# Performance work log

Hardware: AMD Instinct MI355X
Metric: run time of the kernel (lower is better)

The kernel has to match this reference:

```python
import math
import jax, jax.numpy as jnp
import numpy as np

B, L, S, H, E = 4, 2048, 2048, 8, 64

def setup_inputs() -> dict:
    key = jax.random.key(0)
    kq, kk, kv, km = jax.random.split(key, 4)
    queries = jax.random.normal(kq, (B, L, H, E), dtype=jnp.float32)
    keys = jax.random.normal(kk, (B, S, H, E), dtype=jnp.float32)
    values = jax.random.normal(kv, (B, S, H, E), dtype=jnp.float32)
    # bool mask [B, L, S]; True => masked out (filled with -10000)
    attn_mask = jax.random.randint(km, (B, L, S), 0, 2).astype(bool)
    return {"queries": queries, "keys": keys, "values": values, "attn_mask": attn_mask}

def reference(queries, keys, values, attn_mask):
    # queries: [B,L,H,E], keys/values: [B,S,H,E], attn_mask: [B,L,S] bool
    Edim = queries.shape[-1]
    scale = 1.0 / math.sqrt(Edim)  # self.scale is None -> 1/sqrt(E)
    scores = jnp.einsum('blhe,bshe->bhls', queries, keys) * scale  # [B,H,L,S]
    scores = jnp.where(attn_mask[:, None, :, :], jnp.float32(-10000.0), scores)
    A = jax.nn.softmax(scores, axis=-1)  # dropout is identity at eval time
    V = jnp.einsum('bhls,bshd->blhd', A, values)  # [B,L,H,E]
    return V, A
```

## Files before the change

kernel.cpp:

```cpp
#include <hip/hip_runtime.h>


typedef __attribute__((ext_vector_type(8))) short bf16x8;
typedef __attribute__((ext_vector_type(4))) short bf16x4;
typedef __attribute__((ext_vector_type(4))) float f32x4;

#define NB 4
#define NL 2048
#define NS 2048
#define NH 8
#define NE 64
#define SKC 64
#define SCALE 0.125f
#define MBIAS 4.0f

static __device__ __forceinline__ short f2bf(float x) {
  unsigned u = __builtin_bit_cast(unsigned, x);
  u += 0x7fffu + ((u >> 16) & 1u);
  return (short)(u >> 16);
}


__global__ __launch_bounds__(256) void cvt_headmajor(const float* __restrict__ in,
                                                     short* __restrict__ out) {
  long i4 = ((long)blockIdx.x * 256 + threadIdx.x) * 4;
  f32x4 v = *(const f32x4*)(in + i4);
  int e4 = (int)(i4 & 63);
  long r = i4 >> 6;
  int h = (int)(r & 7);
  long r2 = r >> 3;
  int t = (int)(r2 & 2047);
  int b = (int)(r2 >> 11);
  bf16x4 o;
  o[0] = f2bf(v[0]); o[1] = f2bf(v[1]); o[2] = f2bf(v[2]); o[3] = f2bf(v[3]);
  *(bf16x4*)(out + ((((long)b * NH + h) * NL + t) * NE + e4)) = o;
}

__global__ __launch_bounds__(256) void transpose_v(const float* __restrict__ V,
                                                   short* __restrict__ Vt) {
  __shared__ short t_lds[64 * 65];
  const int tid = threadIdx.x;
  const int b = blockIdx.x >> 8;
  const int h = (blockIdx.x >> 5) & 7;
  const int sb = (blockIdx.x & 31) * 64;
  {
    const int s = tid >> 2, e0 = (tid & 3) * 16;
    const float* vp = V + ((((long)b * NS + sb + s) * NH + h) * NE + e0);
    #pragma unroll
    for (int j = 0; j < 4; ++j) {
      f32x4 u = *(const f32x4*)(vp + j * 4);
      #pragma unroll
      for (int r = 0; r < 4; ++r) t_lds[(e0 + j * 4 + r) * 65 + s] = f2bf(u[r]);
    }
  }
  __syncthreads();
  {
    const int e = tid >> 2, s0 = (tid & 3) * 16;
    short* op = Vt + (((long)b * NH + h) * NE + e) * NS + sb + s0;
    short tmp[16];
    #pragma unroll
    for (int j = 0; j < 16; ++j) tmp[j] = t_lds[e * 65 + s0 + j];
    *(bf16x8*)(op)     = *(bf16x8*)(tmp);
    *(bf16x8*)(op + 8) = *(bf16x8*)(tmp + 8);
  }
}

__global__ __launch_bounds__(256) void pack_mask(const int* __restrict__ M,
                                                 unsigned long long* __restrict__ Mb) {
  const long total = (long)NB * NL * NS;
  long g = (long)blockIdx.x * 256 + threadIdx.x;
  const long stride = (long)gridDim.x * 256;
  for (; g < total; g += stride) {
    unsigned long long bal = __ballot(M[g] != 0);
    if ((threadIdx.x & 63) == 0) Mb[g >> 6] = bal;
  }
}


template<int RS>
static __device__ __forceinline__ void stage_tile(const short* __restrict__ base,
                                                  short* lds, int tid, int w) {
  #pragma unroll
  for (int c = 0; c < 2; ++c) {
    const int rr = (tid >> 3) + c * 32;
    const int gg = (tid & 7) ^ (rr & 7);
    const short* sp = base + (long)rr * RS + gg * 8;
    __builtin_amdgcn_global_load_lds(
        (const __attribute__((address_space(1))) void*)sp,
        (__attribute__((address_space(3))) void*)(void*)((char*)lds + c * 4096 + w * 1024),
        16, 0, 0);
  }
}

__global__ __launch_bounds__(256, 2)
void attn_main(const short* __restrict__ Qb, const short* __restrict__ Kb,
               const short* __restrict__ Vt, const unsigned long long* __restrict__ Mb,
               float* __restrict__ OutV, float* __restrict__ OutA)
{
  __shared__ short k_lds[2][SKC * 64];
  __shared__ short vt_lds[2][NE * 64];
  __shared__ short p_lds[4][16 * 64];

  const int bid = blockIdx.x;
  const int hh = bid & 7, qt = (bid >> 3) & 15, bb = bid >> 7;
  const int tid = threadIdx.x, w = tid >> 6, lane = tid & 63;
  const int lq = lane & 15, lg = lane >> 4;
  const int qwA = qt * 128 + w * 16, qrowA = qwA + lq;
  const int qwB = qwA + 64,          qrowB = qrowA + 64;

  const short* Kpan = Kb + (long)(bb * NH + hh) * NS * NE;
  const short* Vpan = Vt + (long)(bb * NH + hh) * NE * NS;

  bf16x8 qfA0, qfA1, qfB0, qfB1;
  {
    const short* qp = Qb + ((long)(bb * NH + hh) * NL + qrowA) * NE + 8 * lg;
    qfA0 = *(const bf16x8*)(qp);
    qfA1 = *(const bf16x8*)(qp + 32);
    qfB0 = *(const bf16x8*)(qp + 64 * NE);
    qfB1 = *(const bf16x8*)(qp + 64 * NE + 32);
  }

  const unsigned long long* mrowA = Mb + ((long)bb * NL + qrowA) * (NS / 64);
  const unsigned long long* mrowB = Mb + ((long)bb * NL + qrowB) * (NS / 64);

  float l0 = 0.f, l1 = 0.f, l2 = 0.f, l3 = 0.f;
  stage_tile<NE>(Kpan, &k_lds[0][0], tid, w);
  __syncthreads();
  unsigned long long mcA = mrowA[0];
  for (int sb = 0; sb < NS; sb += SKC) {
    const int cb = (sb >> 6) & 1;
    if (sb + SKC < NS)
      stage_tile<NE>(Kpan + (long)(sb + SKC) * NE, &k_lds[cb ^ 1][0], tid, w);
    const unsigned long long mnA = (sb + SKC < NS) ? mrowA[(sb >> 6) + 1] : 0ULL;
    #pragma unroll
    for (int st = 0; st < SKC; st += 16) {
      const int krow = st + lq, sw = (krow & 7) << 3;
      const bf16x8 kf0 = *(const bf16x8*)&k_lds[cb][(krow * 64 + 8 * lg) ^ sw];
      const bf16x8 kf1 = *(const bf16x8*)&k_lds[cb][(krow * 64 + 32 + 8 * lg) ^ sw];
      f32x4 c = {0.f, 0.f, 0.f, 0.f};
      c = __builtin_amdgcn_mfma_f32_16x16x32_bf16(kf0, qfA0, c, 0, 0, 0);
      c = __builtin_amdgcn_mfma_f32_16x16x32_bf16(kf1, qfA1, c, 0, 0, 0);
      const unsigned mb4 = (unsigned)(mcA >> (st + 4 * lg)) & 0xFu;
      l0 += (mb4 & 1u) ? 0.f : __expf(fmaf(c[0], SCALE, -MBIAS));
      l1 += (mb4 & 2u) ? 0.f : __expf(fmaf(c[1], SCALE, -MBIAS));
      l2 += (mb4 & 4u) ? 0.f : __expf(fmaf(c[2], SCALE, -MBIAS));
      l3 += (mb4 & 8u) ? 0.f : __expf(fmaf(c[3], SCALE, -MBIAS));
    }
    mcA = mnA;
    __syncthreads();
  }
  float lA = (l0 + l1) + (l2 + l3);
  lA += __shfl_xor(lA, 16, 64);
  lA += __shfl_xor(lA, 32, 64);
  const float rinvA = 1.0f / lA;

  f32x4 accvA[4];
  #pragma unroll
  for (int et = 0; et < 4; ++et) accvA[et] = (f32x4){0.f, 0.f, 0.f, 0.f};
  l0 = l1 = l2 = l3 = 0.f;

  float* arowA = OutA + (((long)(bb * NH + hh)) * NL + qrowA) * NS;

  stage_tile<NE>(Kpan, &k_lds[0][0], tid, w);
  stage_tile<NS>(Vpan, &vt_lds[0][0], tid, w);
  __syncthreads();
  mcA = mrowA[0];
  unsigned long long mcB = mrowB[0];
  for (int sb = 0; sb < NS; sb += SKC) {
    const int cb = (sb >> 6) & 1;
    if (sb + SKC < NS) {
      stage_tile<NE>(Kpan + (long)(sb + SKC) * NE, &k_lds[cb ^ 1][0], tid, w);
      stage_tile<NS>(Vpan + (sb + SKC), &vt_lds[cb ^ 1][0], tid, w);
    }
    const unsigned long long mnA = (sb + SKC < NS) ? mrowA[(sb >> 6) + 1] : 0ULL;
    const unsigned long long mnB = (sb + SKC < NS) ? mrowB[(sb >> 6) + 1] : 0ULL;
    #pragma unroll
    for (int st = 0; st < SKC; st += 16) {
      const int krow = st + lq, sw = (krow & 7) << 3;
      const bf16x8 kf0 = *(const bf16x8*)&k_lds[cb][(krow * 64 + 8 * lg) ^ sw];
      const bf16x8 kf1 = *(const bf16x8*)&k_lds[cb][(krow * 64 + 32 + 8 * lg) ^ sw];
      f32x4 cA = {0.f, 0.f, 0.f, 0.f};
      cA = __builtin_amdgcn_mfma_f32_16x16x32_bf16(kf0, qfA0, cA, 0, 0, 0);
      cA = __builtin_amdgcn_mfma_f32_16x16x32_bf16(kf1, qfA1, cA, 0, 0, 0);
      f32x4 cB = {0.f, 0.f, 0.f, 0.f};
      cB = __builtin_amdgcn_mfma_f32_16x16x32_bf16(kf0, qfB0, cB, 0, 0, 0);
      cB = __builtin_amdgcn_mfma_f32_16x16x32_bf16(kf1, qfB1, cB, 0, 0, 0);
      const unsigned mA4 = (unsigned)(mcA >> (st + 4 * lg)) & 0xFu;
      const float p0 = (mA4 & 1u) ? 0.f : __expf(fmaf(cA[0], SCALE, -MBIAS));
      const float p1 = (mA4 & 2u) ? 0.f : __expf(fmaf(cA[1], SCALE, -MBIAS));
      const float p2 = (mA4 & 4u) ? 0.f : __expf(fmaf(cA[2], SCALE, -MBIAS));
      const float p3 = (mA4 & 8u) ? 0.f : __expf(fmaf(cA[3], SCALE, -MBIAS));
      const float a0 = p0 * rinvA, a1 = p1 * rinvA, a2 = p2 * rinvA, a3 = p3 * rinvA;
      f32x4 av = {a0, a1, a2, a3};
      __builtin_nontemporal_store(av, (f32x4*)(arowA + sb + st + 4 * lg));
      bf16x4 pv;
      pv[0] = f2bf(a0); pv[1] = f2bf(a1); pv[2] = f2bf(a2); pv[3] = f2bf(a3);
      *(bf16x4*)&p_lds[w][(lq * 64 + st + 4 * lg) ^ ((lq & 7) << 3)] = pv;
      const unsigned mB4 = (unsigned)(mcB >> (st + 4 * lg)) & 0xFu;
      l0 += (mB4 & 1u) ? 0.f : __expf(fmaf(cB[0], SCALE, -MBIAS));
      l1 += (mB4 & 2u) ? 0.f : __expf(fmaf(cB[1], SCALE, -MBIAS));
      l2 += (mB4 & 4u) ? 0.f : __expf(fmaf(cB[2], SCALE, -MBIAS));
      l3 += (mB4 & 8u) ? 0.f : __expf(fmaf(cB[3], SCALE, -MBIAS));
    }
    #pragma unroll
    for (int kc2 = 0; kc2 < 2; ++kc2) {
      const bf16x8 pf = *(const bf16x8*)&p_lds[w][(lq * 64 + kc2 * 32 + 8 * lg) ^ ((lq & 7) << 3)];
      #pragma unroll
      for (int et = 0; et < 4; ++et) {
        const int er = et * 16 + lq;
        const bf16x8 vf = *(const bf16x8*)&vt_lds[cb][(er * 64 + kc2 * 32 + 8 * lg) ^ ((er & 7) << 3)];
        accvA[et] = __builtin_amdgcn_mfma_f32_16x16x32_bf16(pf, vf, accvA[et], 0, 0, 0);
      }
    }
    mcA = mnA; mcB = mnB;
    __syncthreads();
  }
  float lB = (l0 + l1) + (l2 + l3);
  lB += __shfl_xor(lB, 16, 64);
  lB += __shfl_xor(lB, 32, 64);
  const float rinvB = 1.0f / lB;

  {
    float* vout = OutV + (((long)bb * NL + qwA + 4 * lg) * NH + hh) * NE + lq;
    #pragma unroll
    for (int r = 0; r < 4; ++r)
      #pragma unroll
      for (int et = 0; et < 4; ++et)
        vout[(long)r * (NH * NE) + et * 16] = accvA[et][r];
  }

  f32x4 accvB[4];
  #pragma unroll
  for (int et = 0; et < 4; ++et) accvB[et] = (f32x4){0.f, 0.f, 0.f, 0.f};

  float* arowB = OutA + (((long)(bb * NH + hh)) * NL + qrowB) * NS;

  stage_tile<NE>(Kpan, &k_lds[0][0], tid, w);
  stage_tile<NS>(Vpan, &vt_lds[0][0], tid, w);
  __syncthreads();
  mcB = mrowB[0];
  for (int sb = 0; sb < NS; sb += SKC) {
    const int cb = (sb >> 6) & 1;
    if (sb + SKC < NS) {
      stage_tile<NE>(Kpan + (long)(sb + SKC) * NE, &k_lds[cb ^ 1][0], tid, w);
      stage_tile<NS>(Vpan + (sb + SKC), &vt_lds[cb ^ 1][0], tid, w);
    }
    const unsigned long long mnB = (sb + SKC < NS) ? mrowB[(sb >> 6) + 1] : 0ULL;
    #pragma unroll
    for (int st = 0; st < SKC; st += 16) {
      const int krow = st + lq, sw = (krow & 7) << 3;
      const bf16x8 kf0 = *(const bf16x8*)&k_lds[cb][(krow * 64 + 8 * lg) ^ sw];
      const bf16x8 kf1 = *(const bf16x8*)&k_lds[cb][(krow * 64 + 32 + 8 * lg) ^ sw];
      f32x4 c = {0.f, 0.f, 0.f, 0.f};
      c = __builtin_amdgcn_mfma_f32_16x16x32_bf16(kf0, qfB0, c, 0, 0, 0);
      c = __builtin_amdgcn_mfma_f32_16x16x32_bf16(kf1, qfB1, c, 0, 0, 0);
      const unsigned mb4 = (unsigned)(mcB >> (st + 4 * lg)) & 0xFu;
      const float p0 = (mb4 & 1u) ? 0.f : __expf(fmaf(c[0], SCALE, -MBIAS));
      const float p1 = (mb4 & 2u) ? 0.f : __expf(fmaf(c[1], SCALE, -MBIAS));
      const float p2 = (mb4 & 4u) ? 0.f : __expf(fmaf(c[2], SCALE, -MBIAS));
      const float p3 = (mb4 & 8u) ? 0.f : __expf(fmaf(c[3], SCALE, -MBIAS));
      const float a0 = p0 * rinvB, a1 = p1 * rinvB, a2 = p2 * rinvB, a3 = p3 * rinvB;
      f32x4 av = {a0, a1, a2, a3};
      __builtin_nontemporal_store(av, (f32x4*)(arowB + sb + st + 4 * lg));
      bf16x4 pv;
      pv[0] = f2bf(a0); pv[1] = f2bf(a1); pv[2] = f2bf(a2); pv[3] = f2bf(a3);
      *(bf16x4*)&p_lds[w][(lq * 64 + st + 4 * lg) ^ ((lq & 7) << 3)] = pv;
    }
    #pragma unroll
    for (int kc2 = 0; kc2 < 2; ++kc2) {
      const bf16x8 pf = *(const bf16x8*)&p_lds[w][(lq * 64 + kc2 * 32 + 8 * lg) ^ ((lq & 7) << 3)];
      #pragma unroll
      for (int et = 0; et < 4; ++et) {
        const int er = et * 16 + lq;
        const bf16x8 vf = *(const bf16x8*)&vt_lds[cb][(er * 64 + kc2 * 32 + 8 * lg) ^ ((er & 7) << 3)];
        accvB[et] = __builtin_amdgcn_mfma_f32_16x16x32_bf16(pf, vf, accvB[et], 0, 0, 0);
      }
    }
    mcB = mnB;
    __syncthreads();
  }

  {
    float* vout = OutV + (((long)bb * NL + qwB + 4 * lg) * NH + hh) * NE + lq;
    #pragma unroll
    for (int r = 0; r < 4; ++r)
      #pragma unroll
      for (int et = 0; et < 4; ++et)
        vout[(long)r * (NH * NE) + et * 16] = accvB[et][r];
  }
}

extern "C" void kernel_launch(void* const* d_in, const int* in_sizes, int n_in,
                              void* d_out, int out_size, void* d_ws, size_t ws_size,
                              hipStream_t stream) {
  const float* Q = (const float*)d_in[0];
  const float* K = (const float*)d_in[1];
  const float* V = (const float*)d_in[2];
  const int*   M = (const int*)d_in[3];
  float* outv = (float*)d_out;
  float* outa = outv + (size_t)NB * NL * NH * NE;

  const size_t NQK = (size_t)NB * NH * NL * NE;
  short* Qb  = (short*)d_ws;
  short* Kbw = Qb + NQK;
  short* Vtw = Kbw + NQK;
  unsigned long long* Mbp = (unsigned long long*)(Vtw + NQK);

  cvt_headmajor<<<dim3((unsigned)(NQK / 4 / 256)), 256, 0, stream>>>(Q, Qb);
  cvt_headmajor<<<dim3((unsigned)(NQK / 4 / 256)), 256, 0, stream>>>(K, Kbw);
  transpose_v<<<dim3(NB * NH * (NS / 64)), 256, 0, stream>>>(V, Vtw);
  pack_mask<<<dim3(2048), 256, 0, stream>>>(M, Mbp);

  attn_main<<<dim3(NB * (NL / 128) * NH), 256, 0, stream>>>(Qb, Kbw, Vtw, Mbp, outv, outa);
}
```

Measured before the change: 213.6 us.

## Fuse preprocessing into one kernel, load Q directly, use exp2

Merges the K conversion, V transpose and mask packing into a single launch partitioned by block index. It drops the separate Q conversion by having the main kernel read fp32 Q and pack it to bf16 in registers. It also replaces __expf with hardware exp2 using pre-scaled log2e constants. The aim is to cut launch overhead and one round trip through memory for Q, at the cost of slightly more register work at the start of the main kernel.

Result: faster. 203.1 us (-4.9%).

```diff
diff --git a/kernel.cpp b/kernel.cpp
--- a/kernel.cpp
+++ b/kernel.cpp
@@ -11,8 +11,9 @@
 #define NH 8
 #define NE 64
 #define SKC 64
-#define SCALE 0.125f
-#define MBIAS 4.0f
+#define SC2 0.18033688011112042f
+#define MB2 -5.770780163555854f
+#define EXP2(x) __builtin_amdgcn_exp2f(x)
 
 static __device__ __forceinline__ short f2bf(float x) {
   unsigned u = __builtin_bit_cast(unsigned, x);
@@ -20,59 +21,64 @@
   return (short)(u >> 16);
 }
 
-
-__global__ __launch_bounds__(256) void cvt_headmajor(const float* __restrict__ in,
-                                                     short* __restrict__ out) {
-  long i4 = ((long)blockIdx.x * 256 + threadIdx.x) * 4;
-  f32x4 v = *(const f32x4*)(in + i4);
-  int e4 = (int)(i4 & 63);
-  long r = i4 >> 6;
-  int h = (int)(r & 7);
-  long r2 = r >> 3;
-  int t = (int)(r2 & 2047);
-  int b = (int)(r2 >> 11);
-  bf16x4 o;
-  o[0] = f2bf(v[0]); o[1] = f2bf(v[1]); o[2] = f2bf(v[2]); o[3] = f2bf(v[3]);
-  *(bf16x4*)(out + ((((long)b * NH + h) * NL + t) * NE + e4)) = o;
-}
-
-__global__ __launch_bounds__(256) void transpose_v(const float* __restrict__ V,
-                                                   short* __restrict__ Vt) {
+static __device__ __forceinline__ bf16x8 pack8(f32x4 a, f32x4 b) {
+  bf16x8 t;
+  t[0] = f2bf(a[0]); t[1] = f2bf(a[1]); t[2] = f2bf(a[2]); t[3] = f2bf(a[3]);
+  t[4] = f2bf(b[0]); t[5] = f2bf(b[1]); t[6] = f2bf(b[2]); t[7] = f2bf(b[3]);
+  return t;
+}
+
+__global__ __launch_bounds__(256)
+void prep_all(const float* __restrict__ K, const float* __restrict__ V,
+              const int* __restrict__ M, short* __restrict__ Kb,
+              short* __restrict__ Vt, unsigned long long* __restrict__ Mb) {
   __shared__ short t_lds[64 * 65];
-  const int tid = threadIdx.x;
-  const int b = blockIdx.x >> 8;
-  const int h = (blockIdx.x >> 5) & 7;
-  const int sb = (blockIdx.x & 31) * 64;
-  {
-    const int s = tid >> 2, e0 = (tid & 3) * 16;
-    const float* vp = V + ((((long)b * NS + sb + s) * NH + h) * NE + e0);
-    #pragma unroll
-    for (int j = 0; j < 4; ++j) {
-      f32x4 u = *(const f32x4*)(vp + j * 4);
-      #pragma unroll
-      for (int r = 0; r < 4; ++r) t_lds[(e0 + j * 4 + r) * 65 + s] = f2bf(u[r]);
-    }
-  }
-  __syncthreads();
-  {
-    const int e = tid >> 2, s0 = (tid & 3) * 16;
-    short* op = Vt + (((long)b * NH + h) * NE + e) * NS + sb + s0;
-    short tmp[16];
-    #pragma unroll
-    for (int j = 0; j < 16; ++j) tmp[j] = t_lds[e * 65 + s0 + j];
-    *(bf16x8*)(op)     = *(bf16x8*)(tmp);
-    *(bf16x8*)(op + 8) = *(bf16x8*)(tmp + 8);
-  }
-}
-
-__global__ __launch_bounds__(256) void pack_mask(const int* __restrict__ M,
-                                                 unsigned long long* __restrict__ Mb) {
-  const long total = (long)NB * NL * NS;
-  long g = (long)blockIdx.x * 256 + threadIdx.x;
-  const long stride = (long)gridDim.x * 256;
-  for (; g < total; g += stride) {
-    unsigned long long bal = __ballot(M[g] != 0);
-    if ((threadIdx.x & 63) == 0) Mb[g >> 6] = bal;
+  const int bid = blockIdx.x, tid = threadIdx.x;
+  if (bid < 4096) {
+    long i4 = ((long)bid * 256 + tid) * 4;
+    f32x4 v = *(const f32x4*)(K + i4);
+    int e4 = (int)(i4 & 63);
+    long r = i4 >> 6;
+    int h = (int)(r & 7);
+    long r2 = r >> 3;
+    int t = (int)(r2 & 2047);
+    int b = (int)(r2 >> 11);
+    bf16x4 o;
+    o[0] = f2bf(v[0]); o[1] = f2bf(v[1]); o[2] = f2bf(v[2]); o[3] = f2bf(v[3]);
+    *(bf16x4*)(Kb + ((((long)b * NH + h) * NL + t) * NE + e4)) = o;
+  } else if (bid < 5120) {
+    const int vb = bid - 4096;
+    const int b = vb >> 8;
+    const int h = (vb >> 5) & 7;
+    const int sb = (vb & 31) * 64;
+    {
+      const int s = tid >> 2, e0 = (tid & 3) * 16;
+      const float* vp = V + ((((long)b * NS + sb + s) * NH + h) * NE + e0);
+      #pragma unroll
+      for (int j = 0; j < 4; ++j) {
+        f32x4 u = *(const f32x4*)(vp + j * 4);
+        #pragma unroll
+        for (int r = 0; r < 4; ++r) t_lds[(e0 + j * 4 + r) * 65 + s] = f2bf(u[r]);
+      }
+    }
+    __syncthreads();
+    {
+      const int e = tid >> 2, s0 = (tid & 3) * 16;
+      short* op = Vt + (((long)b * NH + h) * NE + e) * NS + sb + s0;
+      short tmp[16];
+      #pragma unroll
+      for (int j = 0; j < 16; ++j) tmp[j] = t_lds[e * 65 + s0 + j];
+      *(bf16x8*)(op)     = *(bf16x8*)(tmp);
+      *(bf16x8*)(op + 8) = *(bf16x8*)(tmp + 8);
+    }
+  } else {
+    const long total = (long)NB * NL * NS;
+    long g = (long)(bid - 5120) * 256 + tid;
+    const long stride = 2048L * 256;
+    for (; g < total; g += stride) {
+      unsigned long long bal = __ballot(M[g] != 0);
+      if ((tid & 63) == 0) Mb[g >> 6] = bal;
+    }
   }
 }
 
@@ -93,7 +99,7 @@
 }
 
 __global__ __launch_bounds__(256, 2)
-void attn_main(const short* __restrict__ Qb, const short* __restrict__ Kb,
+void attn_main(const float* __restrict__ Qg, const short* __restrict__ Kb,
                const short* __restrict__ Vt, const unsigned long long* __restrict__ Mb,
                float* __restrict__ OutV, float* __restrict__ OutA)
 {
@@ -113,11 +119,12 @@
 
   bf16x8 qfA0, qfA1, qfB0, qfB1;
   {
-    const short* qp = Qb + ((long)(bb * NH + hh) * NL + qrowA) * NE + 8 * lg;
-    qfA0 = *(const bf16x8*)(qp);
-    qfA1 = *(const bf16x8*)(qp + 32);
-    qfB0 = *(const bf16x8*)(qp + 64 * NE);
-    qfB1 = *(const bf16x8*)(qp + 64 * NE + 32);
+    const float* qp = Qg + (((long)bb * NL + qrowA) * NH + hh) * NE + 8 * lg;
+    qfA0 = pack8(*(const f32x4*)(qp),      *(const f32x4*)(qp + 4));
+    qfA1 = pack8(*(const f32x4*)(qp + 32), *(const f32x4*)(qp + 36));
+    const float* qpB = qp + (long)64 * NH * NE;
+    qfB0 = pack8(*(const f32x4*)(qpB),      *(const f32x4*)(qpB + 4));
+    qfB1 = pack8(*(const f32x4*)(qpB + 32), *(const f32x4*)(qpB + 36));
   }
 
   const unsigned long long* mrowA = Mb + ((long)bb * NL + qrowA) * (NS / 64);
@@ -141,10 +148,10 @@
       c = __builtin_amdgcn_mfma_f32_16x16x32_bf16(kf0, qfA0, c, 0, 0, 0);
       c = __builtin_amdgcn_mfma_f32_16x16x32_bf16(kf1, qfA1, c, 0, 0, 0);
       const unsigned mb4 = (unsigned)(mcA >> (st + 4 * lg)) & 0xFu;
-      l0 += (mb4 & 1u) ? 0.f : __expf(fmaf(c[0], SCALE, -MBIAS));
-      l1 += (mb4 & 2u) ? 0.f : __expf(fmaf(c[1], SCALE, -MBIAS));
-      l2 += (mb4 & 4u) ? 0.f : __expf(fmaf(c[2], SCALE, -MBIAS));
-      l3 += (mb4 & 8u) ? 0.f : __expf(fmaf(c[3], SCALE, -MBIAS));
+      l0 += (mb4 & 1u) ? 0.f : EXP2(fmaf(c[0], SC2, MB2));
+      l1 += (mb4 & 2u) ? 0.f : EXP2(fmaf(c[1], SC2, MB2));
+      l2 += (mb4 & 4u) ? 0.f : EXP2(fmaf(c[2], SC2, MB2));
+      l3 += (mb4 & 8u) ? 0.f : EXP2(fmaf(c[3], SC2, MB2));
     }
     mcA = mnA;
     __syncthreads();
@@ -186,10 +193,10 @@
       cB = __builtin_amdgcn_mfma_f32_16x16x32_bf16(kf0, qfB0, cB, 0, 0, 0);
       cB = __builtin_amdgcn_mfma_f32_16x16x32_bf16(kf1, qfB1, cB, 0, 0, 0);
       const unsigned mA4 = (unsigned)(mcA >> (st + 4 * lg)) & 0xFu;
-      const float p0 = (mA4 & 1u) ? 0.f : __expf(fmaf(cA[0], SCALE, -MBIAS));
-      const float p1 = (mA4 & 2u) ? 0.f : __expf(fmaf(cA[1], SCALE, -MBIAS));
-      const float p2 = (mA4 & 4u) ? 0.f : __expf(fmaf(cA[2], SCALE, -MBIAS));
-      const float p3 = (mA4 & 8u) ? 0.f : __expf(fmaf(cA[3], SCALE, -MBIAS));
+      const float p0 = (mA4 & 1u) ? 0.f : EXP2(fmaf(cA[0], SC2, MB2));
+      const float p1 = (mA4 & 2u) ? 0.f : EXP2(fmaf(cA[1], SC2, MB2));
+      const float p2 = (mA4 & 4u) ? 0.f : EXP2(fmaf(cA[2], SC2, MB2));
+      const float p3 = (mA4 & 8u) ? 0.f : EXP2(fmaf(cA[3], SC2, MB2));
       const float a0 = p0 * rinvA, a1 = p1 * rinvA, a2 = p2 * rinvA, a3 = p3 * rinvA;
       f32x4 av = {a0, a1, a2, a3};
       __builtin_nontemporal_store(av, (f32x4*)(arowA + sb + st + 4 * lg));
@@ -197,10 +204,10 @@
       pv[0] = f2bf(a0); pv[1] = f2bf(a1); pv[2] = f2bf(a2); pv[3] = f2bf(a3);
       *(bf16x4*)&p_lds[w][(lq * 64 + st + 4 * lg) ^ ((lq & 7) << 3)] = pv;
       const unsigned mB4 = (unsigned)(mcB >> (st + 4 * lg)) & 0xFu;
-      l0 += (mB4 & 1u) ? 0.f : __expf(fmaf(cB[0], SCALE, -MBIAS));
-      l1 += (mB4 & 2u) ? 0.f : __expf(fmaf(cB[1], SCALE, -MBIAS));
-      l2 += (mB4 & 4u) ? 0.f : __expf(fmaf(cB[2], SCALE, -MBIAS));
-      l3 += (mB4 & 8u) ? 0.f : __expf(fmaf(cB[3], SCALE, -MBIAS));
+      l0 += (mB4 & 1u) ? 0.f : EXP2(fmaf(cB[0], SC2, MB2));
+      l1 += (mB4 & 2u) ? 0.f : EXP2(fmaf(cB[1], SC2, MB2));
+      l2 += (mB4 & 4u) ? 0.f : EXP2(fmaf(cB[2], SC2, MB2));
+      l3 += (mB4 & 8u) ? 0.f : EXP2(fmaf(cB[3], SC2, MB2));
     }
     #pragma unroll
     for (int kc2 = 0; kc2 < 2; ++kc2) {
@@ -255,10 +262,10 @@
       c = __builtin_amdgcn_mfma_f32_16x16x32_bf16(kf0, qfB0, c, 0, 0, 0);
       c = __builtin_amdgcn_mfma_f32_16x16x32_bf16(kf1, qfB1, c, 0, 0, 0);
       const unsigned mb4 = (unsigned)(mcB >> (st + 4 * lg)) & 0xFu;
-      const float p0 = (mb4 & 1u) ? 0.f : __expf(fmaf(c[0], SCALE, -MBIAS));
-      const float p1 = (mb4 & 2u) ? 0.f : __expf(fmaf(c[1], SCALE, -MBIAS));
-      const float p2 = (mb4 & 4u) ? 0.f : __expf(fmaf(c[2], SCALE, -MBIAS));
-      const float p3 = (mb4 & 8u) ? 0.f : __expf(fmaf(c[3], SCALE, -MBIAS));
+      const float p0 = (mb4 & 1u) ? 0.f : EXP2(fmaf(c[0], SC2, MB2));
+      const float p1 = (mb4 & 2u) ? 0.f : EXP2(fmaf(c[1], SC2, MB2));
+      const float p2 = (mb4 & 4u) ? 0.f : EXP2(fmaf(c[2], SC2, MB2));
+      const float p3 = (mb4 & 8u) ? 0.f : EXP2(fmaf(c[3], SC2, MB2));
       const float a0 = p0 * rinvB, a1 = p1 * rinvB, a2 = p2 * rinvB, a3 = p3 * rinvB;
       f32x4 av = {a0, a1, a2, a3};
       __builtin_nontemporal_store(av, (f32x4*)(arowB + sb + st + 4 * lg));
@@ -301,15 +308,10 @@
   float* outa = outv + (size_t)NB * NL * NH * NE;
 
   const size_t NQK = (size_t)NB * NH * NL * NE;
-  short* Qb  = (short*)d_ws;
-  short* Kbw = Qb + NQK;
+  short* Kbw = (short*)d_ws;
   short* Vtw = Kbw + NQK;
   unsigned long long* Mbp = (unsigned long long*)(Vtw + NQK);
 
-  cvt_headmajor<<<dim3((unsigned)(NQK / 4 / 256)), 256, 0, stream>>>(Q, Qb);
-  cvt_headmajor<<<dim3((unsigned)(NQK / 4 / 256)), 256, 0, stream>>>(K, Kbw);
-  transpose_v<<<dim3(NB * NH * (NS / 64)), 256, 0, stream>>>(V, Vtw);
-  pack_mask<<<dim3(2048), 256, 0, stream>>>(M, Mbp);
-
-  attn_main<<<dim3(NB * (NL / 128) * NH), 256, 0, stream>>>(Qb, Kbw, Vtw, Mbp, outv, outa);
-}
+  prep_all<<<dim3(7168), 256, 0, stream>>>(K, V, M, Kbw, Vtw, Mbp);
+  attn_main<<<dim3(NB * (NL / 128) * NH), 256, 0, stream>>>(Q, Kbw, Vtw, Mbp, outv, outa);
+}
```
